# Kernel tuning notes

Hardware: AMD Instinct MI355X
Metric: run time of the kernel (lower is better)

The kernel has to match this reference:

```python
import jax, jax.numpy as jnp
import numpy as np

B, U, K, N = 32, 4096, 4, 2
K2 = K // 2
STRIDE = 2 * U // K      # per-shard input/hidden width = 2048
UN = U // N              # per-group gate width = 2048


def setup_inputs() -> dict:
    key = jax.random.key(0)
    k0, k1, k2, k3 = jax.random.split(key, 4)
    x = jax.random.normal(k0, (B, U), jnp.float32)
    # h states: n groups, k/2 shards each, each [B, 2U/k]
    hs = jax.random.normal(k1, (N, K2, B, STRIDE), jnp.float32)
    # c states: n groups, k devices each, each [B, U/n]
    cs = jax.random.normal(k2, (N, K, B, UN), jnp.float32)
    # weights: n groups x k shards, each [2U/k, 4U/n] (keras 'uniform' init ~ small)
    ws = jax.random.normal(k3, (N, K, STRIDE, 4 * UN), jnp.float32) * 0.02
    return {"x": x, "hs": hs, "cs": cs, "ws": ws}


def reference(x, hs, cs, ws):
    n, k, d, f4 = ws.shape   # d = 2U/k, f4 = 4U/n
    k2 = k // 2
    b, u = x.shape
    # parallel_matmul: x split into k/2 column chunks, each hit by ws[:, :k/2];
    # the k/2 hidden shards hit ws[:, k/2:]; ring-allreduce == sum of partials.
    x_chunks = x.reshape(b, k2, d)                                  # [B, k/2, 2U/k]
    ifgo = (jnp.einsum('btd,jtdf->jbf', x_chunks, ws[:, :k2])
            + jnp.einsum('jtbd,jtdf->jbf', hs, ws[:, k2:]))         # [n, B, 4U/n]
    i, f, g, o = jnp.split(ifgo, 4, axis=-1)                         # each [n, B, U/n]
    i = jax.nn.sigmoid(i)[:, None]                                   # broadcast over k devices
    f = jax.nn.sigmoid(f)[:, None]
    o = jax.nn.sigmoid(o)[:, None]
    g = jnp.tanh(g)[:, None]
    new_c = f * cs + i * g                                           # [n, k, B, U/n]
    new_h = o * jnp.tanh(new_c)                                      # [n, k, B, U/n]
    # allconcat_ring over the n groups along features: h_full[d] = concat_j new_h[j, d]
    h_full = jnp.transpose(new_h, (1, 2, 0, 3)).reshape(k, b, u)     # [k, B, U]
    x_out = h_full[0]
    # next-step h states: device k/2+t keeps column slice t of width 2U/k
    second = h_full[k2:].reshape(k2, b, k2, u // k2)                 # [k/2, B, k/2, 2U/k]
    idx = jnp.arange(k2)
    h_state = second[idx, :, idx, :]                                 # [k/2, B, 2U/k]
    new_hs = jnp.broadcast_to(h_state[None], (n, k2, b, u // k2))    # replicated per group
    return x_out, new_hs, new_c
```

## Files before the change

### kernel.cpp

```cpp
#include <hip/hip_runtime.h>
#include <hip/hip_bf16.h>
#include <math.h>


#define IN_T_ELEMS (2 * 8192 * 32)
#define NSPLIT 16

__global__ __launch_bounds__(256) void transpose_in(const float* __restrict__ x,
                                                    const float* __restrict__ hs,
                                                    float* __restrict__ in_t) {
    int tid = blockIdx.x * 256 + threadIdx.x;
    int b   = tid & 31;
    int kkd = (tid >> 5) & 8191;
    int j   = tid >> 18;
    float v;
    if (kkd < 4096) {
        v = x[b * 4096 + kkd];
    } else {
        int kk = kkd >> 11;
        int d  = kkd & 2047;
        v = hs[((j * 2 + (kk - 2)) * 32 + b) * 2048 + d];
    }
    in_t[tid] = v;
}

__global__ __launch_bounds__(256, 4) void gemm_partial(const float* __restrict__ in_t,
                                                       const float* __restrict__ wsm,
                                                       float* __restrict__ partial) {
    int lin = blockIdx.x;
    int s   = lin & (NSPLIT - 1);
    int ft  = (lin >> 4) & 31;
    int j   = lin >> 9;
    int w    = __builtin_amdgcn_readfirstlane((int)(threadIdx.x >> 6));
    int lane = threadIdx.x & 63;
    int f0   = ft * 256 + lane * 4;
    int k0   = s * 512;

    const float* __restrict__ wp = wsm + ((size_t)j * 8192 + k0) * 8192 + f0;
    const float* __restrict__ ip = in_t + (size_t)(j * 8192 + k0) * 32 + w * 8;

    float acc[8][4];
#pragma unroll
    for (int b = 0; b < 8; ++b)
#pragma unroll
        for (int q = 0; q < 4; ++q) acc[b][q] = 0.f;

    float4 wa[8], wb[8];
#pragma unroll
    for (int u = 0; u < 8; ++u)
        wa[u] = *(const float4*)(wp + (size_t)u * 8192);
    wp += (size_t)8 * 8192;

#define FMA_BLOCK(WV)                                                  \
    {                                                                  \
        float av[8][8];                                                \
        _Pragma("unroll")                                              \
        for (int u = 0; u < 8; ++u)                                    \
            _Pragma("unroll")                                          \
            for (int b = 0; b < 8; ++b)                                \
                av[u][b] = ip[u * 32 + b];                             \
        _Pragma("unroll")                                              \
        for (int u = 0; u < 8; ++u)                                    \
            _Pragma("unroll")                                          \
            for (int b = 0; b < 8; ++b) {                              \
                acc[b][0] = fmaf(av[u][b], WV[u].x, acc[b][0]);        \
                acc[b][1] = fmaf(av[u][b], WV[u].y, acc[b][1]);        \
                acc[b][2] = fmaf(av[u][b], WV[u].z, acc[b][2]);        \
                acc[b][3] = fmaf(av[u][b], WV[u].w, acc[b][3]);        \
            }                                                          \
        ip += 8 * 32;                                                  \
    }

    for (int t = 0; t < 512; t += 16) {
#pragma unroll
        for (int u = 0; u < 8; ++u)
            wb[u] = *(const float4*)(wp + (size_t)u * 8192);
        wp += (size_t)8 * 8192;
        FMA_BLOCK(wa)
        if (t + 16 < 512) {
#pragma unroll
            for (int u = 0; u < 8; ++u)
                wa[u] = *(const float4*)(wp + (size_t)u * 8192);
            wp += (size_t)8 * 8192;
        }
        FMA_BLOCK(wb)
    }
#undef FMA_BLOCK

    size_t pbase = ((size_t)((j * NSPLIT + s) * 32 + w * 8)) * 8192 + f0;
#pragma unroll
    for (int b = 0; b < 8; ++b)
        *(float4*)(partial + pbase + (size_t)b * 8192) = *(const float4*)acc[b];
}

__device__ __forceinline__ float sigmoidf_(float v) { return 1.f / (1.f + expf(-v)); }

__global__ __launch_bounds__(256) void epilogue(const float* __restrict__ partial,
                                                const float* __restrict__ cs,
                                                float* __restrict__ out) {
    int tid = blockIdx.x * 256 + threadIdx.x;
    int un  = tid & 2047;
    int b   = (tid >> 11) & 31;
    int j   = tid >> 16;

    float g4[4];
#pragma unroll
    for (int gate = 0; gate < 4; ++gate) {
        int f = gate * 2048 + un;
        float sum = 0.f;
#pragma unroll
        for (int s = 0; s < NSPLIT; ++s)
            sum += partial[((size_t)((j * NSPLIT + s) * 32 + b)) * 8192 + f];
        g4[gate] = sum;
    }
    float iv = sigmoidf_(g4[0]);
    float fv = sigmoidf_(g4[1]);
    float gv = tanhf(g4[2]);
    float ov = sigmoidf_(g4[3]);
    float ig = iv * gv;

#pragma unroll
    for (int kk = 0; kk < 4; ++kk) {
        float c_old = cs[((j * 4 + kk) * 32 + b) * 2048 + un];
        float c_new = fv * c_old + ig;
        float h     = ov * tanhf(c_new);
        out[393216 + ((j * 4 + kk) * 32 + b) * 2048 + un] = c_new;
        if (kk == 0) {
            out[b * 4096 + j * 2048 + un] = h;
        }
        if (kk == j + 2) {
            out[131072 + ((0 * 2 + j) * 32 + b) * 2048 + un] = h;
            out[131072 + ((1 * 2 + j) * 32 + b) * 2048 + un] = h;
        }
    }
}

extern "C" void kernel_launch(void* const* d_in, const int* in_sizes, int n_in,
                              void* d_out, int out_size, void* d_ws, size_t ws_size,
                              hipStream_t stream) {
    const float* x   = (const float*)d_in[0];
    const float* hs  = (const float*)d_in[1];
    const float* cs  = (const float*)d_in[2];
    const float* wsm = (const float*)d_in[3];
    float* out = (float*)d_out;

    float* in_t    = (float*)d_ws;
    float* partial = (float*)((char*)d_ws + (size_t)IN_T_ELEMS * 4);

    transpose_in<<<524288 / 256, 256, 0, stream>>>(x, hs, in_t);
    gemm_partial<<<1024, 256, 0, stream>>>(in_t, wsm, partial);
    epilogue<<<131072 / 256, 256, 0, stream>>>(partial, cs, out);
}
```

Measured before the change: 172.4 us.

## Stage activation tiles in double-buffered LDS and shrink weight prefetch groups

```diff
diff --git a/kernel.cpp b/kernel.cpp
--- a/kernel.cpp
+++ b/kernel.cpp
@@ -24,20 +24,58 @@
     in_t[tid] = v;
 }
 
+__device__ __forceinline__ void fma_row(float acc[8][4], float4 a0, float4 a1, float4 wv) {
+    acc[0][0] = fmaf(a0.x, wv.x, acc[0][0]);
+    acc[0][1] = fmaf(a0.x, wv.y, acc[0][1]);
+    acc[0][2] = fmaf(a0.x, wv.z, acc[0][2]);
+    acc[0][3] = fmaf(a0.x, wv.w, acc[0][3]);
+    acc[1][0] = fmaf(a0.y, wv.x, acc[1][0]);
+    acc[1][1] = fmaf(a0.y, wv.y, acc[1][1]);
+    acc[1][2] = fmaf(a0.y, wv.z, acc[1][2]);
+    acc[1][3] = fmaf(a0.y, wv.w, acc[1][3]);
+    acc[2][0] = fmaf(a0.z, wv.x, acc[2][0]);
+    acc[2][1] = fmaf(a0.z, wv.y, acc[2][1]);
+    acc[2][2] = fmaf(a0.z, wv.z, acc[2][2]);
+    acc[2][3] = fmaf(a0.z, wv.w, acc[2][3]);
+    acc[3][0] = fmaf(a0.w, wv.x, acc[3][0]);
+    acc[3][1] = fmaf(a0.w, wv.y, acc[3][1]);
+    acc[3][2] = fmaf(a0.w, wv.z, acc[3][2]);
+    acc[3][3] = fmaf(a0.w, wv.w, acc[3][3]);
+    acc[4][0] = fmaf(a1.x, wv.x, acc[4][0]);
+    acc[4][1] = fmaf(a1.x, wv.y, acc[4][1]);
+    acc[4][2] = fmaf(a1.x, wv.z, acc[4][2]);
+    acc[4][3] = fmaf(a1.x, wv.w, acc[4][3]);
+    acc[5][0] = fmaf(a1.y, wv.x, acc[5][0]);
+    acc[5][1] = fmaf(a1.y, wv.y, acc[5][1]);
+    acc[5][2] = fmaf(a1.y, wv.z, acc[5][2]);
+    acc[5][3] = fmaf(a1.y, wv.w, acc[5][3]);
+    acc[6][0] = fmaf(a1.z, wv.x, acc[6][0]);
+    acc[6][1] = fmaf(a1.z, wv.y, acc[6][1]);
+    acc[6][2] = fmaf(a1.z, wv.z, acc[6][2]);
+    acc[6][3] = fmaf(a1.z, wv.w, acc[6][3]);
+    acc[7][0] = fmaf(a1.w, wv.x, acc[7][0]);
+    acc[7][1] = fmaf(a1.w, wv.y, acc[7][1]);
+    acc[7][2] = fmaf(a1.w, wv.z, acc[7][2]);
+    acc[7][3] = fmaf(a1.w, wv.w, acc[7][3]);
+}
+
 __global__ __launch_bounds__(256, 4) void gemm_partial(const float* __restrict__ in_t,
                                                        const float* __restrict__ wsm,
                                                        float* __restrict__ partial) {
+    __shared__ float lds[2][128][32];
+
     int lin = blockIdx.x;
     int s   = lin & (NSPLIT - 1);
     int ft  = (lin >> 4) & 31;
     int j   = lin >> 9;
     int w    = __builtin_amdgcn_readfirstlane((int)(threadIdx.x >> 6));
     int lane = threadIdx.x & 63;
+    int tid  = threadIdx.x;
     int f0   = ft * 256 + lane * 4;
     int k0   = s * 512;
 
-    const float* __restrict__ wp = wsm + ((size_t)j * 8192 + k0) * 8192 + f0;
-    const float* __restrict__ ip = in_t + (size_t)(j * 8192 + k0) * 32 + w * 8;
+    const float* __restrict__ itb  = in_t + (size_t)(j * 8192 + k0) * 32;
+    const float* __restrict__ wrow = wsm + ((size_t)j * 8192 + k0) * 8192 + f0;
 
     float acc[8][4];
 #pragma unroll
@@ -45,47 +83,67 @@
 #pragma unroll
         for (int q = 0; q < 4; ++q) acc[b][q] = 0.f;
 
-    float4 wa[8], wb[8];
-#pragma unroll
-    for (int u = 0; u < 8; ++u)
-        wa[u] = *(const float4*)(wp + (size_t)u * 8192);
-    wp += (size_t)8 * 8192;
-
-#define FMA_BLOCK(WV)                                                  \
-    {                                                                  \
-        float av[8][8];                                                \
-        _Pragma("unroll")                                              \
-        for (int u = 0; u < 8; ++u)                                    \
-            _Pragma("unroll")                                          \
-            for (int b = 0; b < 8; ++b)                                \
-                av[u][b] = ip[u * 32 + b];                             \
-        _Pragma("unroll")                                              \
-        for (int u = 0; u < 8; ++u)                                    \
-            _Pragma("unroll")                                          \
-            for (int b = 0; b < 8; ++b) {                              \
-                acc[b][0] = fmaf(av[u][b], WV[u].x, acc[b][0]);        \
-                acc[b][1] = fmaf(av[u][b], WV[u].y, acc[b][1]);        \
-                acc[b][2] = fmaf(av[u][b], WV[u].z, acc[b][2]);        \
-                acc[b][3] = fmaf(av[u][b], WV[u].w, acc[b][3]);        \
-            }                                                          \
-        ip += 8 * 32;                                                  \
-    }
-
-    for (int t = 0; t < 512; t += 16) {
-#pragma unroll
-        for (int u = 0; u < 8; ++u)
-            wb[u] = *(const float4*)(wp + (size_t)u * 8192);
-        wp += (size_t)8 * 8192;
-        FMA_BLOCK(wa)
-        if (t + 16 < 512) {
-#pragma unroll
-            for (int u = 0; u < 8; ++u)
-                wa[u] = *(const float4*)(wp + (size_t)u * 8192);
-            wp += (size_t)8 * 8192;
-        }
-        FMA_BLOCK(wb)
-    }
-#undef FMA_BLOCK
+    float4 stg[4];
+#pragma unroll
+    for (int i = 0; i < 4; ++i)
+        stg[i] = *(const float4*)(itb + i * 1024 + tid * 4);
+    float4 wa[4], wb[4];
+#pragma unroll
+    for (int u = 0; u < 4; ++u)
+        wa[u] = *(const float4*)(wrow + (size_t)u * 8192);
+#pragma unroll
+    for (int i = 0; i < 4; ++i)
+        *(float4*)(&lds[0][0][0] + i * 1024 + tid * 4) = stg[i];
+    __syncthreads();
+
+    for (int c = 0; c < 4; ++c) {
+        if (c < 3) {
+            const float* src = itb + (c + 1) * 4096 + tid * 4;
+#pragma unroll
+            for (int i = 0; i < 4; ++i)
+                stg[i] = *(const float4*)(src + i * 1024);
+        }
+        const float* cur = &lds[c & 1][0][0] + w * 8;
+#pragma unroll 1
+        for (int g = 0; g < 16; ++g) {
+            int r = c * 128 + g * 8;
+            {
+                const float* p = wrow + (size_t)(r + 4) * 8192;
+#pragma unroll
+                for (int u = 0; u < 4; ++u)
+                    wb[u] = *(const float4*)(p + (size_t)u * 8192);
+            }
+#pragma unroll
+            for (int u = 0; u < 4; ++u) {
+                const float* ar = cur + (g * 8 + u) * 32;
+                float4 a0 = *(const float4*)ar;
+                float4 a1 = *(const float4*)(ar + 4);
+                fma_row(acc, a0, a1, wa[u]);
+            }
+            {
+                int nr = r + 8;
+                if (nr >= 512) nr = 0;
+                const float* p = wrow + (size_t)nr * 8192;
+#pragma unroll
+                for (int u = 0; u < 4; ++u)
+                    wa[u] = *(const float4*)(p + (size_t)u * 8192);
+            }
+#pragma unroll
+            for (int u = 0; u < 4; ++u) {
+                const float* ar = cur + (g * 8 + 4 + u) * 32;
+                float4 a0 = *(const float4*)ar;
+                float4 a1 = *(const float4*)(ar + 4);
+                fma_row(acc, a0, a1, wb[u]);
+            }
+        }
+        if (c < 3) {
+            float* dst = &lds[(c + 1) & 1][0][0] + tid * 4;
+#pragma unroll
+            for (int i = 0; i < 4; ++i)
+                *(float4*)(dst + i * 1024) = stg[i];
+        }
+        __syncthreads();
+    }
 
     size_t pbase = ((size_t)((j * NSPLIT + s) * 32 + w * 8)) * 8192 + f0;
 #pragma unroll
```

Result: no change. 173.6 us (+0.7%).
